# Kernel optimization log

Measured on AMD Instinct MI355X. Metric: run time of the kernel, lower is better.

## Reference

```python
import jax, jax.numpy as jnp
import numpy as np

H = 32   # num_heads
G = 8    # num_groups (KV heads)
GS = H // G  # group_size
D_MODEL = 2048
HEAD_DIM = D_MODEL // H  # 64


def setup_inputs() -> dict:
    key = jax.random.key(0)
    ks = jax.random.split(key, 9)
    B, S = 2, 2048
    s_in = 1.0 / np.sqrt(D_MODEL)
    return {
        "x": jax.random.normal(ks[0], (B, S, D_MODEL), jnp.float32),
        "Wq": jax.random.normal(ks[1], (D_MODEL, H * HEAD_DIM), jnp.float32) * s_in,
        "bq": jnp.zeros((H * HEAD_DIM,), jnp.float32),
        "Wk": jax.random.normal(ks[2], (D_MODEL, G * HEAD_DIM), jnp.float32) * s_in,
        "bk": jnp.zeros((G * HEAD_DIM,), jnp.float32),
        "Wv": jax.random.normal(ks[3], (D_MODEL, G * HEAD_DIM), jnp.float32) * s_in,
        "bv": jnp.zeros((G * HEAD_DIM,), jnp.float32),
        "Wo": jax.random.normal(ks[4], (H * HEAD_DIM, D_MODEL), jnp.float32) * s_in,
        "bo": jnp.zeros((D_MODEL,), jnp.float32),
    }


def reference(x, Wq, bq, Wk, bk, Wv, bv, Wo, bo):
    B, S, _ = x.shape
    scale = 1.0 / np.sqrt(HEAD_DIM)
    # Projections
    q = (x @ Wq + bq).reshape(B, S, H, HEAD_DIM)          # [B,S,H,D]
    k = (x @ Wk + bk).reshape(B, S, G, HEAD_DIM)          # [B,S,G,D]
    v = (x @ Wv + bv).reshape(B, S, G, HEAD_DIM)
    # Group heads: head h belongs to group h // GS (matches repeat_interleave)
    q = q.reshape(B, S, G, GS, HEAD_DIM).transpose(0, 2, 3, 1, 4)  # [B,G,GS,S,D]
    k = k.transpose(0, 2, 1, 3)                                    # [B,G,S,D]
    v = v.transpose(0, 2, 1, 3)                                    # [B,G,S,D]
    # scores[b,g,m,s,t] = q[b,g,m,s,:] . k[b,g,t,:]
    scores = jnp.einsum('bgmsd,bgtd->bgmst', q, k) * scale
    attn = jax.nn.softmax(scores, axis=-1)
    ctx = jnp.einsum('bgmst,bgtd->bgmsd', attn, v)                 # [B,G,GS,S,D]
    ctx = ctx.transpose(0, 3, 1, 2, 4).reshape(B, S, H * HEAD_DIM)  # [B,S,d_model]
    return ctx @ Wo + bo
```

## Files before the change

kernel.cpp:

```cpp
#include <hip/hip_runtime.h>
#include <stdint.h>

#define DEVINL __device__ __forceinline__

typedef unsigned short u16;
typedef unsigned int   u32;
typedef __attribute__((ext_vector_type(8)))  __bf16 bf16x8;
typedef __attribute__((ext_vector_type(4)))  float  f32x4;
typedef __attribute__((ext_vector_type(16))) float  f32x16;
typedef __attribute__((ext_vector_type(4)))  u32    u32x4;

static constexpr int SEQ    = 2048;
static constexpr int DMODEL = 2048;
static constexpr int NHEAD  = 32;
static constexpr int NGRP   = 8;
static constexpr int DHEAD  = 64;
static constexpr int MTOK   = 2 * SEQ;
static constexpr int NQKV   = NHEAD*DHEAD + 2*NGRP*DHEAD;

DEVINL u16 f2bf(float f) {
  unsigned u = __builtin_bit_cast(unsigned, f);
  u += 0x7fffu + ((u >> 16) & 1u);
  return (u16)(u >> 16);
}

DEVINL void gld16(const void* g, void* l) {
  typedef __attribute__((address_space(1))) const void* gp_t;
  typedef __attribute__((address_space(3))) void* lp_t;
  __builtin_amdgcn_global_load_lds((gp_t)g, (lp_t)l, 16, 0, 0);
}

DEVINL f32x4 mfma16(bf16x8 a, bf16x8 b, f32x4 c) {
  return __builtin_amdgcn_mfma_f32_16x16x32_bf16(a, b, c, 0, 0, 0);
}
DEVINL f32x16 mfma32(bf16x8 a, bf16x8 b, f32x16 c) {
  return __builtin_amdgcn_mfma_f32_32x32x16_bf16(a, b, c, 0, 0, 0);
}
DEVINL u32 cvtpk(float lo, float hi_) {
  u32 r;
  asm("v_cvt_pk_bf16_f32 %0, %1, %2" : "=v"(r) : "v"(lo), "v"(hi_));
  return r;
}
DEVINL void plswap(u32& a, u32& b) {
  asm("v_permlane32_swap_b32 %0, %1" : "+v"(a), "+v"(b));
}

static constexpr float CS = 0.18033688011112042f;

__global__ void k_cvt(const float* __restrict__ s, u16* __restrict__ d) {
  int i = (blockIdx.x * 256 + threadIdx.x) * 4;
  float4 v = *reinterpret_cast<const float4*>(s + i);
  ushort4 o;
  o.x = f2bf(v.x); o.y = f2bf(v.y); o.z = f2bf(v.z); o.w = f2bf(v.w);
  *reinterpret_cast<ushort4*>(d + i) = o;
}

__global__ void k_tconv4(const float* __restrict__ Wq, const float* __restrict__ Wk,
                         const float* __restrict__ Wv, const float* __restrict__ Wo,
                         u16* __restrict__ wqkvT, u16* __restrict__ woT) {
  const int z = blockIdx.z;
  const float* src; u16* dst; int N;
  if      (z == 0) { src = Wq; dst = wqkvT;                          N = 2048; }
  else if (z == 1) { src = Wk; dst = wqkvT + (size_t)2048 * DMODEL;  N = 512;  }
  else if (z == 2) { src = Wv; dst = wqkvT + (size_t)2560 * DMODEL;  N = 512;  }
  else             { src = Wo; dst = woT;                            N = 2048; }
  const int n0 = blockIdx.x * 32;
  if (n0 >= N) return;
  __shared__ float t[32][33];
  const int k0 = blockIdx.y * 32;
  const int tx = threadIdx.x, ty = threadIdx.y;
  #pragma unroll
  for (int r = 0; r < 32; r += 8)
    t[r + ty][tx] = src[(size_t)(k0 + r + ty) * N + n0 + tx];
  __syncthreads();
  #pragma unroll
  for (int r = 0; r < 32; r += 8)
    dst[(size_t)(n0 + r + ty) * DMODEL + k0 + tx] = f2bf(t[tx][r + ty]);
}

__global__ void k_packbias(const float* __restrict__ bq, const float* __restrict__ bk,
                           const float* __restrict__ bv, float* __restrict__ d) {
  int i = blockIdx.x * 256 + threadIdx.x;
  d[i] = i < 2048 ? bq[i] : (i < 2560 ? bk[i - 2048] : bv[i - 2560]);
}

template<int ISV>
__global__ void k_pack(const u16* __restrict__ qkv, u16* __restrict__ out) {
  __shared__ u16 t[64][72];
  const int blk = blockIdx.x;
  const int sblk = blk & 31, g = (blk >> 5) & 7, bb = blk >> 8;
  const int tid = threadIdx.x;
  const size_t srcbase = ((size_t)bb * SEQ + sblk * 64) * NQKV + (ISV ? 2560 : 2048) + g * 64;
  #pragma unroll
  for (int i = 0; i < 2; ++i) {
    int c = tid * 2 + i;
    int row = c >> 3, dc = (c & 7) * 8;
    *(bf16x8*)&t[row][dc] = *(const bf16x8*)(qkv + srcbase + (size_t)row * NQKV + dc);
  }
  __syncthreads();
  const int bg = bb * 8 + g;
  #pragma unroll
  for (int r = 0; r < 2; ++r) {
    int f = tid + 256 * r;
    int lane = f & 63, cj = (f >> 6) & 3, stl = f >> 8;
    int q = lane & 31, hi = lane >> 5;
    size_t o = ((((size_t)bg * 64 + sblk * 2 + stl) * 4 + cj) * 64 + lane) * 8;
    if (ISV) {
      int dcol = (cj & 1) * 32 + q;
      int s0 = stl * 32 + (cj >> 1) * 16 + hi * 8;
      u16 tmp[8];
      #pragma unroll
      for (int e = 0; e < 8; ++e) tmp[e] = t[s0 + e][dcol];
      *(ushort4*)(out + o)     = *(ushort4*)&tmp[0];
      *(ushort4*)(out + o + 4) = *(ushort4*)&tmp[4];
    } else {
      int srow = stl * 32 + q;
      int d0 = cj * 16 + hi * 8;
      *(bf16x8*)(out + o) = *(const bf16x8*)&t[srow][d0];
    }
  }
}

template<int F32OUT, int SCALEQ>
__global__ __launch_bounds__(256, 3)
void k_gemm(const u16* __restrict__ A, const u16* __restrict__ Bt,
            const float* __restrict__ bias, void* __restrict__ Cv,
            int K, int ldc)
{
  __shared__ __align__(16) u16 lA[128 * 32];
  __shared__ __align__(16) u16 lB[128 * 32];
  const int tid = threadIdx.x;
  const int lane = tid & 63, wid = tid >> 6;
  const int fr = lane & 15, fq = lane >> 4;
  const int n0 = blockIdx.x * 128, m0 = blockIdx.y * 128;
  const int wr = wid >> 1, wc = wid & 1;

  f32x4 acc[4][4];
  #pragma unroll
  for (int i = 0; i < 4; ++i)
    #pragma unroll
    for (int j = 0; j < 4; ++j) acc[i][j] = f32x4{0.f, 0.f, 0.f, 0.f};

  const int s0 = (wid * 2 + 0) * 64 + lane;
  const int s1 = (wid * 2 + 1) * 64 + lane;
  const int r0 = s0 >> 2, k0s = 8 * (s0 & 3);
  const int r1 = s1 >> 2, k1s = 8 * (s1 & 3);
  const u16* gA0 = A  + (size_t)(m0 + r0) * K + k0s;
  const u16* gA1 = A  + (size_t)(m0 + r1) * K + k1s;
  const u16* gB0 = Bt + (size_t)(n0 + r0) * K + k0s;
  const u16* gB1 = Bt + (size_t)(n0 + r1) * K + k1s;
  u16* lA0 = &lA[(wid * 2 + 0) * 512];
  u16* lA1 = &lA[(wid * 2 + 1) * 512];
  u16* lB0 = &lB[(wid * 2 + 0) * 512];
  u16* lB1 = &lB[(wid * 2 + 1) * 512];

  int aoff[4], boff[4];
  #pragma unroll
  for (int i = 0; i < 4; ++i) {
    aoff[i] = (wr * 64 + i * 16 + fr) * 64 + fq * 16;
    boff[i] = (wc * 64 + i * 16 + fr) * 64 + fq * 16;
  }
  const char* laB = (const char*)lA;
  const char* lbB = (const char*)lB;

  for (int kt = 0; kt < K; kt += 32) {
    gld16(gA0, lA0); gld16(gA1, lA1);
    gld16(gB0, lB0); gld16(gB1, lB1);
    gA0 += 32; gA1 += 32; gB0 += 32; gB1 += 32;
    __syncthreads();
    bf16x8 a[4], b[4];
    #pragma unroll
    for (int i = 0; i < 4; ++i) a[i] = *(const bf16x8*)(laB + aoff[i]);
    #pragma unroll
    for (int j = 0; j < 4; ++j) b[j] = *(const bf16x8*)(lbB + boff[j]);
    #pragma unroll
    for (int i = 0; i < 4; ++i)
      #pragma unroll
      for (int j = 0; j < 4; ++j)
        acc[i][j] = mfma16(a[i], b[j], acc[i][j]);
    __syncthreads();
  }

  #pragma unroll
  for (int i = 0; i < 4; ++i) {
    const int row = m0 + wr * 64 + i * 16 + fq * 4;
    #pragma unroll
    for (int j = 0; j < 4; ++j) {
      const int col = n0 + wc * 64 + j * 16 + fr;
      const float sc  = (SCALEQ && col < 2048) ? CS : 1.0f;
      const float bvl = bias[col];
      #pragma unroll
      for (int t = 0; t < 4; ++t) {
        const float val = (acc[i][j][t] + bvl) * sc;
        if (F32OUT)
          ((float*)Cv)[(size_t)(row + t) * ldc + col] = val;
        else
          ((u16*)Cv)[(size_t)(row + t) * ldc + col] = f2bf(val);
      }
    }
  }
}

__global__ __launch_bounds__(256, 4)
void k_attn(const u16* __restrict__ qkv, const u16* __restrict__ kswz,
            const u16* __restrict__ vswz, u16* __restrict__ ctx)
{
  __shared__ float lsl[2][64];
  __shared__ float lso[2][32][64];
  const int tid = threadIdx.x, lane = tid & 63, wid = tid >> 6;
  const int q = lane & 31, hi = lane >> 5;
  const int qg = wid >> 1, kvh = wid & 1;
  const int h = blockIdx.y, bb = blockIdx.z, g = h >> 2;
  const int qrow = blockIdx.x * 64 + qg * 32 + q;
  const size_t tokbase = (size_t)bb * SEQ;

  bf16x8 aq[4];
  {
    const u16* qp = qkv + (tokbase + qrow) * NQKV + h * 64 + hi * 8;
    #pragma unroll
    for (int c = 0; c < 4; ++c) aq[c] = *(const bf16x8*)(qp + 16 * c);
  }
  bf16x8 ones;
  #pragma unroll
  for (int e = 0; e < 8; ++e) ones[e] = (__bf16)1.0f;

  f32x16 o0, o1, lac;
  #pragma unroll
  for (int r = 0; r < 16; ++r) { o0[r] = 0.f; o1[r] = 0.f; lac[r] = 0.f; }

  const int bg = bb * 8 + g;
  const u16* kb = kswz + (size_t)bg * 131072 + lane * 8;
  const u16* vb = vswz + (size_t)bg * 131072 + lane * 8;

  const int st0 = kvh * 32, st1 = st0 + 32;

  bf16x8 kf[4];
  #pragma unroll
  for (int c = 0; c < 4; ++c) kf[c] = *(const bf16x8*)(kb + (st0 * 4 + c) * 512);

  for (int st = st0; st < st1; ++st) {
    bf16x8 vf[4];
    #pragma unroll
    for (int j = 0; j < 4; ++j) vf[j] = *(const bf16x8*)(vb + (st * 4 + j) * 512);

    f32x16 s;
    #pragma unroll
    for (int r = 0; r < 16; ++r) s[r] = 0.f;
    __builtin_amdgcn_s_setprio(1);
    #pragma unroll
    for (int c = 0; c < 4; ++c) s = mfma32(kf[c], aq[c], s);
    __builtin_amdgcn_s_setprio(0);

    {
      const int sn = (st + 1 < SEQ / 32) ? st + 1 : st;
      #pragma unroll
      for (int c = 0; c < 4; ++c) kf[c] = *(const bf16x8*)(kb + (sn * 4 + c) * 512);
    }

    float p[16];
    #pragma unroll
    for (int r = 0; r < 16; ++r) p[r] = exp2f(s[r]);

    u32 w0 = cvtpk(p[0],  p[1]),  w1 = cvtpk(p[2],  p[3]);
    u32 w2 = cvtpk(p[4],  p[5]),  w3 = cvtpk(p[6],  p[7]);
    u32 w4 = cvtpk(p[8],  p[9]),  w5 = cvtpk(p[10], p[11]);
    u32 w6 = cvtpk(p[12], p[13]), w7 = cvtpk(p[14], p[15]);
    plswap(w0, w2);  plswap(w1, w3);
    plswap(w4, w6);  plswap(w5, w7);
    u32x4 t0, t1;
    t0.x = w0; t0.y = w1; t0.z = w2; t0.w = w3;
    t1.x = w4; t1.y = w5; t1.z = w6; t1.w = w7;
    bf16x8 pb0 = __builtin_bit_cast(bf16x8, t0);
    bf16x8 pb1 = __builtin_bit_cast(bf16x8, t1);

    __builtin_amdgcn_s_setprio(1);
    o0  = mfma32(vf[0], pb0, o0);
    o1  = mfma32(vf[1], pb0, o1);
    lac = mfma32(ones,  pb0, lac);
    o0  = mfma32(vf[2], pb1, o0);
    o1  = mfma32(vf[3], pb1, o1);
    lac = mfma32(ones,  pb1, lac);
    __builtin_amdgcn_s_setprio(0);
  }

  const float l = lac[0];

  if (kvh == 1) {
    lsl[qg][lane] = l;
    #pragma unroll
    for (int r = 0; r < 16; ++r) {
      lso[qg][r][lane]      = o0[r];
      lso[qg][16 + r][lane] = o1[r];
    }
  }
  __syncthreads();
  if (kvh == 0) {
    const float inv = 1.0f / (l + lsl[qg][lane]);
    u16* cp = ctx + (tokbase + qrow) * DMODEL + h * 64;
    #pragma unroll
    for (int t = 0; t < 4; ++t) {
      ushort4 oa, ob;
      oa.x = f2bf((o0[4*t+0] + lso[qg][4*t+0][lane]) * inv);
      oa.y = f2bf((o0[4*t+1] + lso[qg][4*t+1][lane]) * inv);
      oa.z = f2bf((o0[4*t+2] + lso[qg][4*t+2][lane]) * inv);
      oa.w = f2bf((o0[4*t+3] + lso[qg][4*t+3][lane]) * inv);
      *reinterpret_cast<ushort4*>(cp + 8*t + 4*hi) = oa;
      ob.x = f2bf((o1[4*t+0] + lso[qg][16+4*t+0][lane]) * inv);
      ob.y = f2bf((o1[4*t+1] + lso[qg][16+4*t+1][lane]) * inv);
      ob.z = f2bf((o1[4*t+2] + lso[qg][16+4*t+2][lane]) * inv);
      ob.w = f2bf((o1[4*t+3] + lso[qg][16+4*t+3][lane]) * inv);
      *reinterpret_cast<ushort4*>(cp + 32 + 8*t + 4*hi) = ob;
    }
  }
}

extern "C" void kernel_launch(void* const* d_in, const int* in_sizes, int n_in,
                              void* d_out, int out_size, void* d_ws, size_t ws_size,
                              hipStream_t stream) {
  const float* x  = (const float*)d_in[0];
  const float* Wq = (const float*)d_in[1];
  const float* bq = (const float*)d_in[2];
  const float* Wk = (const float*)d_in[3];
  const float* bk = (const float*)d_in[4];
  const float* Wv = (const float*)d_in[5];
  const float* bv = (const float*)d_in[6];
  const float* Wo = (const float*)d_in[7];
  const float* bo = (const float*)d_in[8];

  char* ws = (char*)d_ws;
  size_t off = 0;
  auto take = [&](size_t bytes) { char* p = ws + off; off += (bytes + 255) & ~(size_t)255; return p; };
  u16*   xb    = (u16*)  take((size_t)MTOK * DMODEL * 2);
  u16*   wqkvT = (u16*)  take((size_t)NQKV * DMODEL * 2);
  u16*   woT   = (u16*)  take((size_t)DMODEL * DMODEL * 2);
  u16*   qkv   = (u16*)  take((size_t)MTOK * NQKV * 2);
  u16*   kswz  = (u16*)  take((size_t)16 * 131072 * 2);
  u16*   vswz  = (u16*)  take((size_t)16 * 131072 * 2);
  float* bqkv  = (float*)take((size_t)NQKV * 4);

  if (off > ws_size) {
    hipMemsetAsync(d_out, 0, (size_t)out_size * 4, stream);
    return;
  }

  dim3 tb(32, 8);
  k_cvt<<<(MTOK * DMODEL) / (4 * 256), 256, 0, stream>>>(x, xb);
  k_tconv4<<<dim3(64, 64, 4), tb, 0, stream>>>(Wq, Wk, Wv, Wo, wqkvT, woT);
  k_packbias<<<NQKV / 256, 256, 0, stream>>>(bq, bk, bv, bqkv);

  k_gemm<0, 1><<<dim3(NQKV / 128, MTOK / 128), 256, 0, stream>>>(
      xb, wqkvT, bqkv, qkv, DMODEL, NQKV);

  k_pack<0><<<512, 256, 0, stream>>>(qkv, kswz);
  k_pack<1><<<512, 256, 0, stream>>>(qkv, vswz);

  u16* ctxb = xb;
  k_attn<<<dim3(SEQ / 64, NHEAD, 2), 256, 0, stream>>>(qkv, kswz, vswz, ctxb);

  k_gemm<1, 0><<<dim3(DMODEL / 128, MTOK / 128), 256, 0, stream>>>(
      ctxb, woT, bo, d_out, DMODEL, DMODEL);
}
```

Baseline: 247.1 us.

## Fuse K/V swizzle packing into QKV projection GEMM epilogue

The QKV projection GEMM epilogue now writes K and V directly into the swizzled MFMA-friendly layouts used by attention, which removes the two separate k_pack kernel launches and their extra read/write pass over the K/V data. The attention loop is also simplified to use incrementing pointers and a hoisted zero accumulator, and the next-K prefetch no longer clamps. The scattered epilogue stores (2-byte writes for K) may be poorly coalesced. The unclamped prefetch reads one tile past the end for the last block.

Result: faster. 241.8 us (-2.2%).

```diff
diff --git a/kernel.cpp b/kernel.cpp
--- a/kernel.cpp
+++ b/kernel.cpp
@@ -84,48 +84,11 @@
   d[i] = i < 2048 ? bq[i] : (i < 2560 ? bk[i - 2048] : bv[i - 2560]);
 }
 
-template<int ISV>
-__global__ void k_pack(const u16* __restrict__ qkv, u16* __restrict__ out) {
-  __shared__ u16 t[64][72];
-  const int blk = blockIdx.x;
-  const int sblk = blk & 31, g = (blk >> 5) & 7, bb = blk >> 8;
-  const int tid = threadIdx.x;
-  const size_t srcbase = ((size_t)bb * SEQ + sblk * 64) * NQKV + (ISV ? 2560 : 2048) + g * 64;
-  #pragma unroll
-  for (int i = 0; i < 2; ++i) {
-    int c = tid * 2 + i;
-    int row = c >> 3, dc = (c & 7) * 8;
-    *(bf16x8*)&t[row][dc] = *(const bf16x8*)(qkv + srcbase + (size_t)row * NQKV + dc);
-  }
-  __syncthreads();
-  const int bg = bb * 8 + g;
-  #pragma unroll
-  for (int r = 0; r < 2; ++r) {
-    int f = tid + 256 * r;
-    int lane = f & 63, cj = (f >> 6) & 3, stl = f >> 8;
-    int q = lane & 31, hi = lane >> 5;
-    size_t o = ((((size_t)bg * 64 + sblk * 2 + stl) * 4 + cj) * 64 + lane) * 8;
-    if (ISV) {
-      int dcol = (cj & 1) * 32 + q;
-      int s0 = stl * 32 + (cj >> 1) * 16 + hi * 8;
-      u16 tmp[8];
-      #pragma unroll
-      for (int e = 0; e < 8; ++e) tmp[e] = t[s0 + e][dcol];
-      *(ushort4*)(out + o)     = *(ushort4*)&tmp[0];
-      *(ushort4*)(out + o + 4) = *(ushort4*)&tmp[4];
-    } else {
-      int srow = stl * 32 + q;
-      int d0 = cj * 16 + hi * 8;
-      *(bf16x8*)(out + o) = *(const bf16x8*)&t[srow][d0];
-    }
-  }
-}
-
-template<int F32OUT, int SCALEQ>
+template<int PROJ>
 __global__ __launch_bounds__(256, 3)
 void k_gemm(const u16* __restrict__ A, const u16* __restrict__ Bt,
             const float* __restrict__ bias, void* __restrict__ Cv,
-            int K, int ldc)
+            u16* __restrict__ kswz, u16* __restrict__ vswz, int K, int ldc)
 {
   __shared__ __align__(16) u16 lA[128 * 32];
   __shared__ __align__(16) u16 lB[128 * 32];
@@ -187,15 +150,41 @@
     #pragma unroll
     for (int j = 0; j < 4; ++j) {
       const int col = n0 + wc * 64 + j * 16 + fr;
-      const float sc  = (SCALEQ && col < 2048) ? CS : 1.0f;
       const float bvl = bias[col];
-      #pragma unroll
-      for (int t = 0; t < 4; ++t) {
-        const float val = (acc[i][j][t] + bvl) * sc;
-        if (F32OUT)
-          ((float*)Cv)[(size_t)(row + t) * ldc + col] = val;
-        else
-          ((u16*)Cv)[(size_t)(row + t) * ldc + col] = f2bf(val);
+      if (PROJ) {
+        if (col < 2048) {
+          #pragma unroll
+          for (int t = 0; t < 4; ++t)
+            ((u16*)Cv)[(size_t)(row + t) * ldc + col] = f2bf((acc[i][j][t] + bvl) * CS);
+        } else if (col < 2560) {
+          const int b  = row >> 11, s = row & 2047;
+          const int g  = (col - 2048) >> 6, d = (col - 2048) & 63;
+          const int bg = b * 8 + g;
+          const int st = s >> 5;
+          const int cj = d >> 4, hi = (d >> 3) & 1, e = d & 7;
+          const size_t base = ((size_t)((bg * 64 + st) * 4 + cj) * 64 + hi * 32 + (s & 31)) * 8 + e;
+          #pragma unroll
+          for (int t = 0; t < 4; ++t)
+            kswz[base + (size_t)t * 8] = f2bf(acc[i][j][t] + bvl);
+        } else {
+          const int b  = row >> 11, s = row & 2047;
+          const int g  = (col - 2560) >> 6, d = (col - 2560) & 63;
+          const int bg = b * 8 + g;
+          const int st = s >> 5;
+          const int cj = ((s >> 4) & 1) * 2 + (d >> 5);
+          const int hi = (s >> 3) & 1, e0 = s & 7;
+          ushort4 pk;
+          pk.x = f2bf(acc[i][j].x + bvl);
+          pk.y = f2bf(acc[i][j].y + bvl);
+          pk.z = f2bf(acc[i][j].z + bvl);
+          pk.w = f2bf(acc[i][j].w + bvl);
+          *reinterpret_cast<ushort4*>(
+            &vswz[((size_t)((bg * 64 + st) * 4 + cj) * 64 + hi * 32 + (d & 31)) * 8 + e0]) = pk;
+        }
+      } else {
+        #pragma unroll
+        for (int t = 0; t < 4; ++t)
+          ((float*)Cv)[(size_t)(row + t) * ldc + col] = acc[i][j][t] + bvl;
       }
     }
   }
@@ -223,39 +212,38 @@
   bf16x8 ones;
   #pragma unroll
   for (int e = 0; e < 8; ++e) ones[e] = (__bf16)1.0f;
+  f32x16 z16;
+  #pragma unroll
+  for (int r = 0; r < 16; ++r) z16[r] = 0.f;
 
   f32x16 o0, o1, lac;
   #pragma unroll
   for (int r = 0; r < 16; ++r) { o0[r] = 0.f; o1[r] = 0.f; lac[r] = 0.f; }
 
   const int bg = bb * 8 + g;
-  const u16* kb = kswz + (size_t)bg * 131072 + lane * 8;
-  const u16* vb = vswz + (size_t)bg * 131072 + lane * 8;
-
-  const int st0 = kvh * 32, st1 = st0 + 32;
+  const int st0 = kvh * 32;
+  const u16* kp = kswz + (size_t)bg * 131072 + (size_t)st0 * 2048 + lane * 8;
+  const u16* vp = vswz + (size_t)bg * 131072 + (size_t)st0 * 2048 + lane * 8;
 
   bf16x8 kf[4];
   #pragma unroll
-  for (int c = 0; c < 4; ++c) kf[c] = *(const bf16x8*)(kb + (st0 * 4 + c) * 512);
-
-  for (int st = st0; st < st1; ++st) {
+  for (int c = 0; c < 4; ++c) kf[c] = *(const bf16x8*)(kp + c * 512);
+
+  for (int it = 0; it < 32; ++it) {
     bf16x8 vf[4];
     #pragma unroll
-    for (int j = 0; j < 4; ++j) vf[j] = *(const bf16x8*)(vb + (st * 4 + j) * 512);
-
-    f32x16 s;
-    #pragma unroll
-    for (int r = 0; r < 16; ++r) s[r] = 0.f;
+    for (int j = 0; j < 4; ++j) vf[j] = *(const bf16x8*)(vp + j * 512);
+
     __builtin_amdgcn_s_setprio(1);
-    #pragma unroll
-    for (int c = 0; c < 4; ++c) s = mfma32(kf[c], aq[c], s);
+    f32x16 s = mfma32(kf[0], aq[0], z16);
+    s = mfma32(kf[1], aq[1], s);
+    s = mfma32(kf[2], aq[2], s);
+    s = mfma32(kf[3], aq[3], s);
     __builtin_amdgcn_s_setprio(0);
 
-    {
-      const int sn = (st + 1 < SEQ / 32) ? st + 1 : st;
-      #pragma unroll
-      for (int c = 0; c < 4; ++c) kf[c] = *(const bf16x8*)(kb + (sn * 4 + c) * 512);
-    }
+    #pragma unroll
+    for (int c = 0; c < 4; ++c) kf[c] = *(const bf16x8*)(kp + 2048 + c * 512);
+    kp += 2048; vp += 2048;
 
     float p[16];
     #pragma unroll
@@ -348,15 +336,12 @@
   k_tconv4<<<dim3(64, 64, 4), tb, 0, stream>>>(Wq, Wk, Wv, Wo, wqkvT, woT);
   k_packbias<<<NQKV / 256, 256, 0, stream>>>(bq, bk, bv, bqkv);
 
-  k_gemm<0, 1><<<dim3(NQKV / 128, MTOK / 128), 256, 0, stream>>>(
-      xb, wqkvT, bqkv, qkv, DMODEL, NQKV);
-
-  k_pack<0><<<512, 256, 0, stream>>>(qkv, kswz);
-  k_pack<1><<<512, 256, 0, stream>>>(qkv, vswz);
+  k_gemm<1><<<dim3(NQKV / 128, MTOK / 128), 256, 0, stream>>>(
+      xb, wqkvT, bqkv, qkv, kswz, vswz, DMODEL, NQKV);
 
   u16* ctxb = xb;
   k_attn<<<dim3(SEQ / 64, NHEAD, 2), 256, 0, stream>>>(qkv, kswz, vswz, ctxb);
 
-  k_gemm<1, 0><<<dim3(DMODEL / 128, MTOK / 128), 256, 0, stream>>>(
-      ctxb, woT, bo, d_out, DMODEL, DMODEL);
-}
+  k_gemm<0><<<dim3(DMODEL / 128, MTOK / 128), 256, 0, stream>>>(
+      ctxb, woT, bo, d_out, nullptr, nullptr, DMODEL, DMODEL);
+}
```
